# Kernel optimization log

Measured on AMD Instinct MI355X. Metric: run time of the kernel, lower is better.

Reference implementation:

```python
import jax, jax.numpy as jnp
import numpy as np

VOCAB = 50000
OOV = 1000
EMB = 256
H = 512          # decoder hidden
ENC = 512        # 2 * encoder_hidden (bidirectional)
B, S, T = 32, 256, 8
NEG = -1e20


def setup_inputs() -> dict:
    key = jax.random.key(0)
    ks = jax.random.split(key, 16)
    inp = {
        'dec_x': jax.random.randint(ks[0], (B, T), 0, VOCAB),
        'enc_x_with_oov': jax.random.randint(ks[1], (B, S), 0, VOCAB + OOV),
        'enc_len': jax.random.randint(ks[2], (B,), 64, S + 1),
        'enc_output': jax.random.normal(ks[3], (B, S, ENC), jnp.float32),
        'enc_h': jax.random.normal(ks[4], (B, H), jnp.float32),
        'enc_c': jax.random.normal(ks[5], (B, H), jnp.float32),
        'batch_size': B,
        'dec_len': T,
        # learned parameters
        'embedding': jax.random.normal(ks[6], (VOCAB, EMB), jnp.float32) * 0.02,
        'lstm_k': jax.random.normal(ks[7], (EMB, 4 * H), jnp.float32) * 0.02,
        'lstm_r': jax.random.normal(ks[8], (H, 4 * H), jnp.float32) * 0.02,
        'lstm_b': jnp.zeros((4 * H,), jnp.float32),
        'attn_w': jax.random.normal(ks[9], (H, ENC), jnp.float32) * 0.02,
        'out_w': jax.random.normal(ks[10], (ENC + H, H), jnp.float32) * 0.02,
        'out_b': jnp.zeros((H,), jnp.float32),
        'gen_w': jax.random.normal(ks[11], (H, VOCAB), jnp.float32) * 0.02,
        'copy_w': jax.random.normal(ks[12], (ENC, H), jnp.float32) * 0.02,
        'copy_b': jnp.zeros((H,), jnp.float32),
    }
    return inp


def _lstm(x, h0, c0, Wk, Wr, b):
    # x: [B, T, E] -> hidden states [B, T, H], final (h, c)
    def step(carry, x_t):
        h, c = carry
        z = x_t @ Wk + h @ Wr + b  # [B, 4H]
        i, f, g, o = jnp.split(z, 4, axis=-1)
        c = jax.nn.sigmoid(f) * c + jax.nn.sigmoid(i) * jnp.tanh(g)
        h = jax.nn.sigmoid(o) * jnp.tanh(c)
        return (h, c), h
    (h, c), hs = jax.lax.scan(step, (h0, c0), jnp.swapaxes(x, 0, 1))
    return jnp.swapaxes(hs, 0, 1), h, c


def reference(dec_x, enc_x_with_oov, enc_len, enc_output, enc_h, enc_c,
              batch_size, dec_len, embedding, lstm_k, lstm_r, lstm_b,
              attn_w, out_w, out_b, gen_w, copy_w, copy_b):
    mask = jnp.arange(S) < enc_len[:, None]          # [B, S] True = keep

    embed_dec = embedding[dec_x]                      # [B, T, E]
    hidden, state_h, state_c = _lstm(embed_dec, enc_h, enc_c, lstm_k, lstm_r, lstm_b)

    # attention ('general' score)
    q = hidden @ attn_w                               # [B, T, ENC]
    scores = jnp.einsum('bte,bse->bts', q, enc_output)
    scores = jnp.where(mask[:, None, :], scores, NEG)
    attn = jax.nn.softmax(scores, axis=2)             # [B, T, S]
    context = jnp.einsum('bts,bse->bte', attn, enc_output)
    attn_out = jnp.tanh(jnp.concatenate([context, hidden], axis=-1) @ out_w + out_b)  # [B, T, H]

    # generation scores, padded with tiny constant for OOV slots
    gen = jnp.exp(attn_out @ gen_w)                   # [B, T, VOCAB]
    gen = jnp.pad(gen, ((0, 0), (0, 0), (0, OOV)), constant_values=1e-10)

    # copy scores scattered into extended vocab
    k = jnp.tanh(enc_output @ copy_w + copy_b)        # [B, S, H]
    cs = jnp.einsum('bsh,bth->bts', k, attn_out)      # [B, T, S]
    cs = jnp.exp(jnp.where(mask[:, None, :], cs, NEG))
    Vt = VOCAB + OOV
    copy_vocab = jnp.zeros((B, T, Vt), cs.dtype).at[
        jnp.arange(B)[:, None, None],
        jnp.arange(T)[None, :, None],
        enc_x_with_oov[:, None, :],
    ].add(cs)                                         # scatter-add, dup indices sum

    total = gen + copy_vocab
    total_prob = jnp.log(total / jnp.sum(total, axis=2, keepdims=True))
    return total_prob, state_h, state_c
```

## Files before the change

### kernel.cpp

```cpp
#include <hip/hip_runtime.h>
#include <hip/hip_bf16.h>

typedef unsigned short u16;
typedef unsigned int   u32;
typedef __attribute__((ext_vector_type(4))) float f4v;
typedef __attribute__((ext_vector_type(8))) short s8v;
typedef __attribute__((ext_vector_type(4))) unsigned int u4v;

#define NB   32
#define NS   256
#define NT   8
#define NH   512
#define NENC 512
#define NEMB 256
#define NVOC 50000
#define NVT  51000

__device__ __forceinline__ float bf2f(u16 u){ return __uint_as_float(((u32)u)<<16); }
__device__ __forceinline__ u16 f2bf(float f){
  u32 x = __float_as_uint(f);
  return (u16)((x + 0x7fffu + ((x>>16)&1u)) >> 16);
}
__device__ __forceinline__ s8v ld_frag16(const u16* p){
  union{ s8v v; u4v u; } t;
  t.u = *(const u4v*)p;
  return t.v;
}
__device__ __forceinline__ f4v mfma16(s8v a, s8v b, f4v c){
  return __builtin_amdgcn_mfma_f32_16x16x32_bf16(a,b,c,0,0,0);
}
__device__ __forceinline__ float sigm(float x){ return 1.f/(1.f+__expf(-x)); }

__global__ __launch_bounds__(256)
void transpose_cvt(const float* __restrict__ in, u16* __restrict__ out,
                   int K, int N)
{
  in  += (size_t)blockIdx.z * K * N;
  out += (size_t)blockIdx.z * K * N;
  __shared__ u16 tile[32*40];
  const int n0 = blockIdx.x*32, k0 = blockIdx.y*32;
  const int tid = threadIdx.x;
  {
    int r = tid>>3, c4 = tid&7;
    int c = n0 + c4*4;
    if (c+4 > N) c = N-4;
    f4v v = *(const f4v*)(in + (size_t)(k0+r)*N + c);
    uint2 p;
    p.x = (u32)f2bf(v.x) | ((u32)f2bf(v.y)<<16);
    p.y = (u32)f2bf(v.z) | ((u32)f2bf(v.w)<<16);
    *(uint2*)&tile[r*40 + c4*4] = p;
  }
  __syncthreads();
  {
    int r2 = tid>>3, kc = tid&7;
    int n = n0 + r2;
    if (n < N){
      u16 e[4];
      #pragma unroll
      for (int j=0; j<4; ++j) e[j] = tile[(kc*4+j)*40 + r2];
      *(uint2*)(out + (size_t)n*K + k0 + kc*4) = *(uint2*)e;
    }
  }
}

__global__ __launch_bounds__(256)
void cvt_bf16(const float* __restrict__ src, u16* __restrict__ dst){
  int i = (blockIdx.x*256 + threadIdx.x) * 4;
  f4v v = *(const f4v*)(src + i);
  uint2 p;
  p.x = (u32)f2bf(v.x) | ((u32)f2bf(v.y)<<16);
  p.y = (u32)f2bf(v.z) | ((u32)f2bf(v.w)<<16);
  *(uint2*)(dst + i) = p;
}

template<int BM, int BN, int EPI, bool ABF16, bool AGATHER, bool MXA>
__global__ __launch_bounds__(256)
void gemm_bt(const void* __restrict__ Av, const u16* __restrict__ Bt,
             float* __restrict__ C, const int* __restrict__ a_idx,
             const float* __restrict__ bias, float* __restrict__ rowsum,
             int K, int lda, int ldc, int nlim)
{
  constexpr int LDT = 40;
  constexpr int PA  = ABF16 ? BM/64 : BM/32;
  constexpr int PB  = BN/64;
  __shared__ u16 Al[2][BM*LDT];
  __shared__ u16 Bl[2][BN*LDT];
  const int tid  = threadIdx.x;
  const int lane = tid & 63;
  const int wave = tid >> 6;
  const int m0 = (MXA ? blockIdx.x : blockIdx.y) * BM;
  const int n0 = (MXA ? blockIdx.y : blockIdx.x) * BN;
  constexpr int TM = BM/32;
  constexpr int TN = BN/32;
  const int wm = (wave>>1)*(BM/2);
  const int wn = (wave&1)*(BN/2);
  const int q  = lane >> 4;
  const int ln = lane & 15;

  const u16*  aS16[PA];
  const float* aS32[PA];
  int aOff[PA];
  if (ABF16){
    const u16* Ag = (const u16*)Av;
    #pragma unroll
    for (int p=0; p<PA; ++p){
      int el = tid + p*256, row = el>>2, ck = el&3;
      aS16[p] = Ag + (size_t)(m0+row)*lda + ck*8;
      aS32[p] = nullptr;
      aOff[p] = row*LDT + ck*8;
    }
  } else {
    const float* Ag = (const float*)Av;
    #pragma unroll
    for (int p=0; p<PA; ++p){
      int el = tid + p*256, row = el>>3, ck = el&7;
      int grow = AGATHER ? a_idx[m0+row] : (m0+row);
      aS32[p] = Ag + (size_t)grow*lda + ck*4;
      aS16[p] = nullptr;
      aOff[p] = row*LDT + ck*4;
    }
  }
  const u16* bS[PB];
  int bOff[PB];
  #pragma unroll
  for (int p=0; p<PB; ++p){
    int el = tid + p*256, row = el>>2, ck = el&3;
    int nr = n0 + row; if (nr >= nlim) nr = nlim-1;
    bS[p]   = Bt + (size_t)nr*K + ck*8;
    bOff[p] = row*LDT + ck*8;
  }

  f4v acc[TM][TN];
  #pragma unroll
  for (int im=0; im<TM; ++im)
    #pragma unroll
    for (int in=0; in<TN; ++in) acc[im][in] = 0.f;

  u4v aR[PA]; f4v aF[PA]; u4v bR[PB];
  if (ABF16){
    #pragma unroll
    for (int p=0; p<PA; ++p) aR[p] = *(const u4v*)(aS16[p]);
  } else {
    #pragma unroll
    for (int p=0; p<PA; ++p) aF[p] = *(const f4v*)(aS32[p]);
  }
  #pragma unroll
  for (int p=0; p<PB; ++p) bR[p] = *(const u4v*)(bS[p]);

  const int KB = K >> 5;
  int cur = 0;
  for (int kb=0; kb<KB; ++kb){
    if (ABF16){
      #pragma unroll
      for (int p=0; p<PA; ++p) *(u4v*)&Al[cur][aOff[p]] = aR[p];
    } else {
      #pragma unroll
      for (int p=0; p<PA; ++p){
        uint2 pk;
        pk.x = (u32)f2bf(aF[p].x) | ((u32)f2bf(aF[p].y)<<16);
        pk.y = (u32)f2bf(aF[p].z) | ((u32)f2bf(aF[p].w)<<16);
        *(uint2*)&Al[cur][aOff[p]] = pk;
      }
    }
    #pragma unroll
    for (int p=0; p<PB; ++p) *(u4v*)&Bl[cur][bOff[p]] = bR[p];
    if (kb+1 < KB){
      const int ko = (kb+1)*32;
      if (ABF16){
        #pragma unroll
        for (int p=0; p<PA; ++p) aR[p] = *(const u4v*)(aS16[p] + ko);
      } else {
        #pragma unroll
        for (int p=0; p<PA; ++p) aF[p] = *(const f4v*)(aS32[p] + ko);
      }
      #pragma unroll
      for (int p=0; p<PB; ++p) bR[p] = *(const u4v*)(bS[p] + ko);
    }
    __syncthreads();
    s8v af[TM], bfr[TN];
    #pragma unroll
    for (int im=0; im<TM; ++im)
      af[im] = ld_frag16(&Al[cur][(wm+im*16+ln)*LDT + q*8]);
    #pragma unroll
    for (int in=0; in<TN; ++in)
      bfr[in] = ld_frag16(&Bl[cur][(wn+in*16+ln)*LDT + q*8]);
    #pragma unroll
    for (int im=0; im<TM; ++im)
      #pragma unroll
      for (int in=0; in<TN; ++in)
        acc[im][in] = mfma16(af[im], bfr[in], acc[im][in]);
    cur ^= 1;
  }

  #pragma unroll
  for (int im=0; im<TM; ++im){
    const int rbase = m0 + wm + im*16 + q*4;
    #pragma unroll
    for (int in=0; in<TN; ++in){
      const int col = n0 + wn + in*16 + ln;
      if (EPI == 0){
        #pragma unroll
        for (int r=0; r<4; ++r)
          C[(size_t)(rbase+r)*ldc + col] = acc[im][in][r];
      } else if (EPI == 1){
        float bb = bias[col];
        u16* Cb = (u16*)C;
        #pragma unroll
        for (int r=0; r<4; ++r)
          Cb[(size_t)(rbase+r)*ldc + col] = f2bf(tanhf(acc[im][in][r] + bb));
      } else if (EPI == 3){
        u16* Cb = (u16*)C;
        #pragma unroll
        for (int r=0; r<4; ++r)
          Cb[(size_t)(rbase+r)*ldc + col] = f2bf(acc[im][in][r]);
      }
    }
  }
}

__global__ __launch_bounds__(256, 3)
void gen_nat(const u16* __restrict__ A,
             const float* __restrict__ W,
             float* __restrict__ outp)
{
  constexpr int LDT = 40;
  __shared__ u16 Al[2][256*LDT];
  __shared__ u16 Bl[2][64*LDT];
  const int tid  = threadIdx.x;
  const int lane = tid & 63, wave = tid >> 6;
  const int q = lane >> 4, ln = lane & 15;
  const int wm = (wave >> 1) * 128;
  const int wn = (wave & 1) * 32;
  const int n0 = blockIdx.x * 64;

  const int arow = tid >> 2, ack = (tid & 3) * 8;
  const int kp = tid >> 4;
  const int nw = tid & 15;
  int bcol = n0 + nw*4; if (bcol > NVOC-4) bcol = NVOC-4;
  const float* w0 = W + (size_t)(2*kp)  *NVOC + bcol;
  const float* w1 = W + (size_t)(2*kp+1)*NVOC + bcol;
  const int bLoff = (nw*4)*LDT + kp*2;
  const size_t CH = (size_t)32*NVOC;

  f4v acc[8][2];
  #pragma unroll
  for (int im=0; im<8; ++im){ acc[im][0] = 0.f; acc[im][1] = 0.f; }

  u4v aA[4], aB[4];
  f4v b0A, b1A, b0B, b1B;
  #pragma unroll
  for (int p=0; p<4; ++p)
    aA[p] = *(const u4v*)(A + (size_t)(arow + p*64)*NH + ack);
  b0A = *(const f4v*)(w0);
  b1A = *(const f4v*)(w1);
  #pragma unroll
  for (int p=0; p<4; ++p)
    aB[p] = *(const u4v*)(A + (size_t)(arow + p*64)*NH + 32 + ack);
  b0B = *(const f4v*)(w0 + CH);
  b1B = *(const f4v*)(w1 + CH);

  for (int kb=0; kb<16; kb+=2){
    #pragma unroll
    for (int p=0; p<4; ++p) *(u4v*)&Al[0][(arow + p*64)*LDT + ack] = aA[p];
    #pragma unroll
    for (int i=0; i<4; ++i){
      u32 v = (u32)f2bf(b0A[i]) | ((u32)f2bf(b1A[i])<<16);
      *(u32*)&Bl[0][bLoff + i*LDT] = v;
    }
    if (kb+2 < 16){
      #pragma unroll
      for (int p=0; p<4; ++p)
        aA[p] = *(const u4v*)(A + (size_t)(arow + p*64)*NH + (kb+2)*32 + ack);
      b0A = *(const f4v*)(w0 + (size_t)(kb+2)*CH);
      b1A = *(const f4v*)(w1 + (size_t)(kb+2)*CH);
    }
    __syncthreads();
    {
      s8v bf0 = ld_frag16(&Bl[0][(wn + ln)*LDT + q*8]);
      s8v bf1 = ld_frag16(&Bl[0][(wn + 16 + ln)*LDT + q*8]);
      #pragma unroll
      for (int im=0; im<8; ++im){
        s8v af = ld_frag16(&Al[0][(wm + im*16 + ln)*LDT + q*8]);
        acc[im][0] = mfma16(af, bf0, acc[im][0]);
        acc[im][1] = mfma16(af, bf1, acc[im][1]);
      }
    }
    #pragma unroll
    for (int p=0; p<4; ++p) *(u4v*)&Al[1][(arow + p*64)*LDT + ack] = aB[p];
    #pragma unroll
    for (int i=0; i<4; ++i){
      u32 v = (u32)f2bf(b0B[i]) | ((u32)f2bf(b1B[i])<<16);
      *(u32*)&Bl[1][bLoff + i*LDT] = v;
    }
    if (kb+3 < 16){
      #pragma unroll
      for (int p=0; p<4; ++p)
        aB[p] = *(const u4v*)(A + (size_t)(arow + p*64)*NH + (kb+3)*32 + ack);
      b0B = *(const f4v*)(w0 + (size_t)(kb+3)*CH);
      b1B = *(const f4v*)(w1 + (size_t)(kb+3)*CH);
    }
    __syncthreads();
    {
      s8v bf0 = ld_frag16(&Bl[1][(wn + ln)*LDT + q*8]);
      s8v bf1 = ld_frag16(&Bl[1][(wn + 16 + ln)*LDT + q*8]);
      #pragma unroll
      for (int im=0; im<8; ++im){
        s8v af = ld_frag16(&Al[1][(wm + im*16 + ln)*LDT + q*8]);
        acc[im][0] = mfma16(af, bf0, acc[im][0]);
        acc[im][1] = mfma16(af, bf1, acc[im][1]);
      }
    }
  }

  #pragma unroll
  for (int im=0; im<8; ++im){
    const int rbase = wm + im*16 + q*4;
    #pragma unroll
    for (int in=0; in<2; ++in){
      const int col = n0 + wn + in*16 + ln;
      if (col < NVT){
        #pragma unroll
        for (int r=0; r<4; ++r){
          float v = (col < NVOC) ? __expf(acc[im][in][r]) : 1e-10f;
          outp[(size_t)(rbase+r)*NVT + col] = v;
        }
      }
    }
  }
}

__global__ __launch_bounds__(256)
void lstm_step2(const u16* __restrict__ wrT, const float* __restrict__ xk,
                const float* __restrict__ bias, const u16* __restrict__ hb_in,
                u16* __restrict__ hb_out, float* __restrict__ c_cur,
                float* __restrict__ concat, float* __restrict__ out_h,
                float* __restrict__ out_c, int t)
{
  const int tid = threadIdx.x, lane = tid & 63, g = tid >> 6;
  const int q = lane >> 4, ln = lane & 15;
  const int j0 = blockIdx.x * 16;

  f4v acc0 = 0.f, acc1 = 0.f;
  const u16* bp = wrT + (size_t)(g*NH + j0 + ln)*NH;
  const u16* a0 = hb_in + (size_t)ln*NH;
  const u16* a1 = hb_in + (size_t)(16+ln)*NH;
  #pragma unroll 4
  for (int kb=0; kb<16; ++kb){
    s8v bf  = ld_frag16(bp + kb*32 + q*8);
    s8v af0 = ld_frag16(a0 + kb*32 + q*8);
    s8v af1 = ld_frag16(a1 + kb*32 + q*8);
    acc0 = mfma16(af0, bf, acc0);
    acc1 = mfma16(af1, bf, acc1);
  }

  __shared__ float zs[4][32][17];
  #pragma unroll
  for (int r=0; r<4; ++r){
    zs[g][q*4+r][ln]    = acc0[r];
    zs[g][16+q*4+r][ln] = acc1[r];
  }
  __syncthreads();

  #pragma unroll
  for (int pp=0; pp<2; ++pp){
    int pair = tid + pp*256;
    int b = pair >> 4, jj = pair & 15;
    int j = j0 + jj;
    const float* xr = xk + (size_t)(b*NT+t)*2048;
    float zi = zs[0][b][jj] + xr[j]        + bias[j];
    float zf = zs[1][b][jj] + xr[NH+j]     + bias[NH+j];
    float zg = zs[2][b][jj] + xr[2*NH+j]   + bias[2*NH+j];
    float zo = zs[3][b][jj] + xr[3*NH+j]   + bias[3*NH+j];
    float c = sigm(zf)*c_cur[(size_t)b*NH+j] + sigm(zi)*tanhf(zg);
    float h = sigm(zo)*tanhf(c);
    c_cur[(size_t)b*NH+j] = c;
    hb_out[(size_t)b*NH+j] = f2bf(h);
    concat[(size_t)(b*NT+t)*1024 + 512 + j] = h;
    if (t == NT-1){ out_h[(size_t)b*NH+j] = h; out_c[(size_t)b*NH+j] = c; }
  }
}

__global__ __launch_bounds__(512)
void attn_sm(const u16* __restrict__ q_bf,
             const u16* __restrict__ enc_bf,
             const int* __restrict__ enc_len,
             float* __restrict__ at_p)
{
  const int b = blockIdx.x;
  __shared__ u16 Al[16*520];
  __shared__ float at[8][256];
  const int tid = threadIdx.x;
  for (int i=tid; i<16*64; i+=512){
    int row = i >> 6, ck = i & 63;
    uint2 v0 = {0u,0u}, v1 = {0u,0u};
    if (row < NT){
      const u16* s = q_bf + ((size_t)(b*NT+row))*NH + ck*8;
      v0 = *(const uint2*)s; v1 = *(const uint2*)(s+4);
    }
    u16* d = &Al[row*520 + ck*8];
    *(uint2*)d = v0; *(uint2*)(d+4) = v1;
  }
  __syncthreads();
  const int wave = tid >> 6, lane = tid & 63;
  const int q = lane >> 4, ln = lane & 15;
  const int len = enc_len[b];
  f4v acc0 = 0.f, acc1 = 0.f;
  const u16* Bg0 = enc_bf + ((size_t)(b*NS + wave*32 + ln))*NENC;
  const u16* Bg1 = enc_bf + ((size_t)(b*NS + wave*32 + 16 + ln))*NENC;
  for (int kb=0; kb<16; ++kb){
    s8v a  = ld_frag16(&Al[ln*520 + kb*32 + q*8]);
    s8v b0 = ld_frag16(Bg0 + kb*32 + q*8);
    s8v b1 = ld_frag16(Bg1 + kb*32 + q*8);
    acc0 = mfma16(a, b0, acc0);
    acc1 = mfma16(a, b1, acc1);
  }
  {
    const int s0 = wave*32 + ln, s1 = s0 + 16;
    const bool m0 = s0 < len, m1 = s1 < len;
    #pragma unroll
    for (int r=0; r<4; ++r){
      int t = q*4 + r;
      if (t < NT){
        at[t][s0] = m0 ? acc0[r] : -3.0e38f;
        at[t][s1] = m1 ? acc1[r] : -3.0e38f;
      }
    }
  }
  __syncthreads();
  {
    float v[4]; float mx = -3.0e38f;
    #pragma unroll
    for (int i=0;i<4;++i){ v[i] = at[wave][lane+64*i]; mx = fmaxf(mx, v[i]); }
    #pragma unroll
    for (int off=1; off<64; off<<=1) mx = fmaxf(mx, __shfl_xor(mx, off, 64));
    float sum = 0.f;
    #pragma unroll
    for (int i=0;i<4;++i){ v[i] = __expf(v[i]-mx); sum += v[i]; }
    #pragma unroll
    for (int off=1; off<64; off<<=1) sum += __shfl_xor(sum, off, 64);
    float inv = 1.f/sum;
    #pragma unroll
    for (int i=0;i<4;++i)
      at_p[((size_t)(b*NT+wave))*NS + lane+64*i] = v[i]*inv;
  }
}

__global__ __launch_bounds__(256)
void attn_ctx2(const float* __restrict__ at_p,
               const u16* __restrict__ encT_bf,
               float* __restrict__ concat)
{
  const int b = blockIdx.x, eb = blockIdx.y;
  __shared__ u16 Al[16*264];
  const int tid = threadIdx.x;
  for (int i=tid; i<16*64; i+=256){
    int row = i >> 6, c4 = i & 63;
    uint2 pk = {0u,0u};
    if (row < NT){
      f4v v = *(const f4v*)(at_p + ((size_t)(b*NT+row))*NS + c4*4);
      pk.x = (u32)f2bf(v.x) | ((u32)f2bf(v.y)<<16);
      pk.y = (u32)f2bf(v.z) | ((u32)f2bf(v.w)<<16);
    }
    *(uint2*)&Al[row*264 + c4*4] = pk;
  }
  __syncthreads();
  const int wave = tid >> 6, lane = tid & 63;
  const int q = lane >> 4, ln = lane & 15;
  const int e = eb*64 + wave*16 + ln;
  f4v acc = 0.f;
  const u16* Bg = encT_bf + ((size_t)(b*NENC + e))*NS;
  for (int kb=0; kb<8; ++kb){
    s8v a  = ld_frag16(&Al[ln*264 + kb*32 + q*8]);
    s8v bb = ld_frag16(Bg + kb*32 + q*8);
    acc = mfma16(a, bb, acc);
  }
  #pragma unroll
  for (int r=0; r<4; ++r){
    int t = q*4 + r;
    if (t < NT) concat[(size_t)(b*NT+t)*1024 + e] = acc[r];
  }
}

__global__ __launch_bounds__(256)
void cs_scatter(const u16* __restrict__ attn_bf, const u16* __restrict__ copy_k,
                const int* __restrict__ enc_x, const int* __restrict__ enc_len,
                float* __restrict__ outp)
{
  const int b  = blockIdx.x >> 2;
  const int sb = blockIdx.x & 3;
  __shared__ u16 Al[16*520];
  const int tid = threadIdx.x;
  for (int i=tid; i<16*64; i+=256){
    int row = i >> 6, ck = i & 63;
    uint2 v0 = {0u,0u}, v1 = {0u,0u};
    if (row < NT){
      const u16* s = attn_bf + ((size_t)(b*NT+row))*NH + ck*8;
      v0 = *(const uint2*)s; v1 = *(const uint2*)(s+4);
    }
    u16* d = &Al[row*520 + ck*8];
    *(uint2*)d = v0; *(uint2*)(d+4) = v1;
  }
  __syncthreads();
  const int wave = tid >> 6, lane = tid & 63;
  const int q = lane >> 4, ln = lane & 15;
  const int s0 = sb*64 + wave*16;
  f4v acc = 0.f;
  const u16* Bg = copy_k + ((size_t)(b*NS + s0 + ln))*NH;
  for (int kb=0; kb<16; ++kb){
    s8v a  = ld_frag16(&Al[ln*520 + kb*32 + q*8]);
    s8v bb = ld_frag16(Bg + kb*32 + q*8);
    acc = mfma16(a, bb, acc);
  }
  const int s = s0 + ln;
  const int len = enc_len[b];
  const int vidx = enc_x[b*NS + s];
  const bool valid = (s < len);
  #pragma unroll
  for (int r=0; r<4; ++r){
    int t = q*4 + r;
    float e = (valid && t < NT) ? __expf(acc[r]) : 0.f;
    if (e != 0.f) atomicAdd(&outp[(size_t)(b*NT+t)*NVT + vidx], e);
  }
}

__global__ __launch_bounds__(256)
void row_reduce_log(const float* __restrict__ outp, float* __restrict__ logsum)
{
  const int r = blockIdx.x;
  const int tid = threadIdx.x;
  const float* p = outp + (size_t)r*NVT;
  float sum = 0.f;
  for (int i4 = tid; i4 < 12750; i4 += 256){
    f4v v = *(const f4v*)(p + i4*4);
    sum += v.x + v.y + v.z + v.w;
  }
  #pragma unroll
  for (int off=1; off<64; off<<=1) sum += __shfl_xor(sum, off, 64);
  __shared__ float ws[4];
  if ((tid & 63) == 0) ws[tid>>6] = sum;
  __syncthreads();
  if (tid == 0) logsum[r] = __logf(ws[0]+ws[1]+ws[2]+ws[3]);
}

__global__ __launch_bounds__(256)
void norm_log(float* __restrict__ outp, const float* __restrict__ logsum){
  const int i4 = blockIdx.x*256 + threadIdx.x;
  if (i4 >= 12750) return;
  const int r = blockIdx.y;
  const float ls = logsum[r];
  float* p = outp + (size_t)r*NVT + i4*4;
  f4v v = *(const f4v*)p;
  v.x = __logf(v.x) - ls;
  v.y = __logf(v.y) - ls;
  v.z = __logf(v.z) - ls;
  v.w = __logf(v.w) - ls;
  *(f4v*)p = v;
}

extern "C" void kernel_launch(void* const* d_in, const int* in_sizes, int n_in,
                              void* d_out, int out_size, void* d_ws, size_t ws_size,
                              hipStream_t stream)
{
  (void)in_sizes; (void)n_in; (void)out_size; (void)ws_size;
  const int*   dec_x      = (const int*)  d_in[0];
  const int*   enc_x      = (const int*)  d_in[1];
  const int*   enc_len    = (const int*)  d_in[2];
  const float* enc_output = (const float*)d_in[3];
  const float* enc_h      = (const float*)d_in[4];
  const float* enc_c      = (const float*)d_in[5];
  const float* embedding  = (const float*)d_in[8];
  const float* lstm_k     = (const float*)d_in[9];
  const float* lstm_r     = (const float*)d_in[10];
  const float* lstm_b     = (const float*)d_in[11];
  const float* attn_w     = (const float*)d_in[12];
  const float* out_w      = (const float*)d_in[13];
  const float* out_b      = (const float*)d_in[14];
  const float* gen_w      = (const float*)d_in[15];
  const float* copy_w     = (const float*)d_in[16];
  const float* copy_b     = (const float*)d_in[17];

  float* outp  = (float*)d_out;
  float* out_h = outp + (size_t)NB*NT*NVT;
  float* out_c = out_h + NB*NH;

  char* ws = (char*)d_ws;
  u16*   wrT     = (u16*)ws;    ws += (size_t)2048*NH*2;
  u16*   lstmkT  = (u16*)ws;    ws += (size_t)2048*NEMB*2;
  u16*   attnT   = (u16*)ws;    ws += (size_t)NENC*NH*2;
  u16*   outT    = (u16*)ws;    ws += (size_t)NH*1024*2;
  u16*   copyT   = (u16*)ws;    ws += (size_t)NH*NENC*2;
  float* xk      = (float*)ws;  ws += (size_t)NB*NT*2048*4;
  u16*   hb0     = (u16*)ws;    ws += (size_t)NB*NH*2;
  u16*   hb1     = (u16*)ws;    ws += (size_t)NB*NH*2;
  float* c_cur   = (float*)ws;  ws += (size_t)NB*NH*4;
  u16*   q_bf    = (u16*)ws;    ws += (size_t)NB*NT*NENC*2;
  float* at_p    = (float*)ws;  ws += (size_t)NB*NT*NS*4;
  float* concat  = (float*)ws;  ws += (size_t)NB*NT*1024*4;
  u16*   attn_bf = (u16*)ws;    ws += (size_t)NB*NT*NH*2;
  u16*   copy_k  = (u16*)ws;    ws += (size_t)NB*NS*NH*2;
  u16*   enc_bf  = (u16*)ws;    ws += (size_t)NB*NS*NENC*2;
  u16*   encT_bf = (u16*)ws;    ws += (size_t)NB*NENC*NS*2;
  float* logsum  = (float*)ws;  ws += NB*NT*4;

  cvt_bf16<<<4096,256,0,stream>>>(enc_output, enc_bf);
  transpose_cvt<<<dim3(16,8,32),256,0,stream>>>(enc_output, encT_bf, NS, NENC);
  transpose_cvt<<<dim3(64,16), 256,0,stream>>>(lstm_r, wrT,    NH,  2048);
  transpose_cvt<<<dim3(64,8),  256,0,stream>>>(lstm_k, lstmkT, NEMB,2048);
  transpose_cvt<<<dim3(16,16), 256,0,stream>>>(attn_w, attnT,  NH,  NENC);
  transpose_cvt<<<dim3(16,32), 256,0,stream>>>(out_w,  outT,   1024,NH);
  transpose_cvt<<<dim3(16,16), 256,0,stream>>>(copy_w, copyT,  NENC,NH);
  cvt_bf16<<<16,256,0,stream>>>(enc_h, hb0);
  hipMemcpyAsync(c_cur, enc_c, NB*NH*4, hipMemcpyDeviceToDevice, stream);

  gemm_bt<64,128,1,true,false,false><<<dim3(4,128),256,0,stream>>>(
      enc_bf, copyT, (float*)copy_k, nullptr, copy_b, nullptr, NENC, NENC, NH, NH);

  gemm_bt<32,64,0,false,true,true><<<dim3(8,32),256,0,stream>>>(
      embedding, lstmkT, xk, dec_x, nullptr, nullptr, NEMB, NEMB, 2048, 2048);

  u16* hb[2] = {hb0, hb1};
  for (int t=0; t<NT; ++t)
    lstm_step2<<<32,256,0,stream>>>(wrT, xk, lstm_b, hb[t&1], hb[(t+1)&1],
                                    c_cur, concat, out_h, out_c, t);

  gemm_bt<32,64,3,false,false,true><<<dim3(8,8),256,0,stream>>>(
      concat + 512, attnT, (float*)q_bf, nullptr, nullptr, nullptr, NH, 1024, NENC, NENC);

  attn_sm<<<32,512,0,stream>>>(q_bf, enc_bf, enc_len, at_p);
  attn_ctx2<<<dim3(32,8),256,0,stream>>>(at_p, encT_bf, concat);

  gemm_bt<32,64,1,false,false,true><<<dim3(8,8),256,0,stream>>>(
      concat, outT, (float*)attn_bf, nullptr, out_b, nullptr, 1024, 1024, NH, NH);

  gen_nat<<<797,256,0,stream>>>(attn_bf, gen_w, outp);

  cs_scatter<<<128,256,0,stream>>>(attn_bf, copy_k, enc_x, enc_len, outp);
  row_reduce_log<<<NB*NT,256,0,stream>>>(outp, logsum);
  norm_log<<<dim3(50,NB*NT),256,0,stream>>>(outp, logsum);
}
```

Measured before the change: 451.6 us.

## Fuse row-sum into gen/copy epilogues, merge weight transposes, drop LDS A staging

```diff
diff --git a/kernel.cpp b/kernel.cpp
--- a/kernel.cpp
+++ b/kernel.cpp
@@ -31,15 +31,11 @@
 }
 __device__ __forceinline__ float sigm(float x){ return 1.f/(1.f+__expf(-x)); }
 
-__global__ __launch_bounds__(256)
-void transpose_cvt(const float* __restrict__ in, u16* __restrict__ out,
-                   int K, int N)
-{
-  in  += (size_t)blockIdx.z * K * N;
-  out += (size_t)blockIdx.z * K * N;
-  __shared__ u16 tile[32*40];
-  const int n0 = blockIdx.x*32, k0 = blockIdx.y*32;
-  const int tid = threadIdx.x;
+__device__ __forceinline__ void transpose_body(const float* in, u16* out,
+                                               int K, int N, int bx, int by,
+                                               int tid, u16* tile)
+{
+  const int n0 = bx*32, k0 = by*32;
   {
     int r = tid>>3, c4 = tid&7;
     int c = n0 + c4*4;
@@ -61,6 +57,35 @@
       *(uint2*)(out + (size_t)n*K + k0 + kc*4) = *(uint2*)e;
     }
   }
+}
+
+__global__ __launch_bounds__(256)
+void transpose_cvt(const float* __restrict__ in, u16* __restrict__ out,
+                   int K, int N)
+{
+  __shared__ u16 tile[32*40];
+  in  += (size_t)blockIdx.z * K * N;
+  out += (size_t)blockIdx.z * K * N;
+  transpose_body(in, out, K, N, blockIdx.x, blockIdx.y, threadIdx.x, tile);
+}
+
+__global__ __launch_bounds__(256)
+void prep_weights(const float* __restrict__ lstm_r, u16* __restrict__ wrT,
+                  const float* __restrict__ lstm_k, u16* __restrict__ lstmkT,
+                  const float* __restrict__ attn_w, u16* __restrict__ attnT,
+                  const float* __restrict__ out_w,  u16* __restrict__ outT,
+                  const float* __restrict__ copy_w, u16* __restrict__ copyT)
+{
+  __shared__ u16 tile[32*40];
+  const int bid = blockIdx.x;
+  const float* in; u16* out; int K, N, nx, lid;
+  if (bid < 1024)      { in=lstm_r; out=wrT;    K=512;  N=2048; nx=64; lid=bid; }
+  else if (bid < 1536) { in=lstm_k; out=lstmkT; K=256;  N=2048; nx=64; lid=bid-1024; }
+  else if (bid < 1792) { in=attn_w; out=attnT;  K=512;  N=512;  nx=16; lid=bid-1536; }
+  else if (bid < 2304) { in=out_w;  out=outT;   K=1024; N=512;  nx=16; lid=bid-1792; }
+  else                 { in=copy_w; out=copyT;  K=512;  N=512;  nx=16; lid=bid-2304; }
+  int bx = lid % nx, by = lid / nx;
+  transpose_body(in, out, K, N, bx, by, threadIdx.x, tile);
 }
 
 __global__ __launch_bounds__(256)
@@ -218,13 +243,12 @@
   }
 }
 
-__global__ __launch_bounds__(256, 3)
+__global__ __launch_bounds__(256, 4)
 void gen_nat(const u16* __restrict__ A,
              const float* __restrict__ W,
-             float* __restrict__ outp)
+             float* __restrict__ outp, float* __restrict__ rowsum)
 {
   constexpr int LDT = 40;
-  __shared__ u16 Al[2][256*LDT];
   __shared__ u16 Bl[2][64*LDT];
   const int tid  = threadIdx.x;
   const int lane = tid & 63, wave = tid >> 6;
@@ -233,44 +257,37 @@
   const int wn = (wave & 1) * 32;
   const int n0 = blockIdx.x * 64;
 
-  const int arow = tid >> 2, ack = (tid & 3) * 8;
   const int kp = tid >> 4;
   const int nw = tid & 15;
   int bcol = n0 + nw*4; if (bcol > NVOC-4) bcol = NVOC-4;
   const float* w0 = W + (size_t)(2*kp)  *NVOC + bcol;
   const float* w1 = W + (size_t)(2*kp+1)*NVOC + bcol;
-  const int bLoff = (nw*4)*LDT + kp*2;
+  const int bRow = nw*4;
   const size_t CH = (size_t)32*NVOC;
 
+  const u16* aP[8];
+  #pragma unroll
+  for (int im=0; im<8; ++im)
+    aP[im] = A + (size_t)(wm + im*16 + ln)*NH;
+
   f4v acc[8][2];
   #pragma unroll
   for (int im=0; im<8; ++im){ acc[im][0] = 0.f; acc[im][1] = 0.f; }
 
-  u4v aA[4], aB[4];
   f4v b0A, b1A, b0B, b1B;
-  #pragma unroll
-  for (int p=0; p<4; ++p)
-    aA[p] = *(const u4v*)(A + (size_t)(arow + p*64)*NH + ack);
   b0A = *(const f4v*)(w0);
   b1A = *(const f4v*)(w1);
-  #pragma unroll
-  for (int p=0; p<4; ++p)
-    aB[p] = *(const u4v*)(A + (size_t)(arow + p*64)*NH + 32 + ack);
   b0B = *(const f4v*)(w0 + CH);
   b1B = *(const f4v*)(w1 + CH);
 
   for (int kb=0; kb<16; kb+=2){
     #pragma unroll
-    for (int p=0; p<4; ++p) *(u4v*)&Al[0][(arow + p*64)*LDT + ack] = aA[p];
-    #pragma unroll
-    for (int i=0; i<4; ++i){
+    for (int j=0; j<4; ++j){
+      int i = (j + nw) & 3;
       u32 v = (u32)f2bf(b0A[i]) | ((u32)f2bf(b1A[i])<<16);
-      *(u32*)&Bl[0][bLoff + i*LDT] = v;
+      *(u32*)&Bl[0][(bRow + i)*LDT + kp*2] = v;
     }
     if (kb+2 < 16){
-      #pragma unroll
-      for (int p=0; p<4; ++p)
-        aA[p] = *(const u4v*)(A + (size_t)(arow + p*64)*NH + (kb+2)*32 + ack);
       b0A = *(const f4v*)(w0 + (size_t)(kb+2)*CH);
       b1A = *(const f4v*)(w1 + (size_t)(kb+2)*CH);
     }
@@ -280,22 +297,18 @@
       s8v bf1 = ld_frag16(&Bl[0][(wn + 16 + ln)*LDT + q*8]);
       #pragma unroll
       for (int im=0; im<8; ++im){
-        s8v af = ld_frag16(&Al[0][(wm + im*16 + ln)*LDT + q*8]);
+        s8v af = ld_frag16(aP[im] + kb*32 + q*8);
         acc[im][0] = mfma16(af, bf0, acc[im][0]);
         acc[im][1] = mfma16(af, bf1, acc[im][1]);
       }
     }
     #pragma unroll
-    for (int p=0; p<4; ++p) *(u4v*)&Al[1][(arow + p*64)*LDT + ack] = aB[p];
-    #pragma unroll
-    for (int i=0; i<4; ++i){
+    for (int j=0; j<4; ++j){
+      int i = (j + nw) & 3;
       u32 v = (u32)f2bf(b0B[i]) | ((u32)f2bf(b1B[i])<<16);
-      *(u32*)&Bl[1][bLoff + i*LDT] = v;
+      *(u32*)&Bl[1][(bRow + i)*LDT + kp*2] = v;
     }
     if (kb+3 < 16){
-      #pragma unroll
-      for (int p=0; p<4; ++p)
-        aB[p] = *(const u4v*)(A + (size_t)(arow + p*64)*NH + (kb+3)*32 + ack);
       b0B = *(const f4v*)(w0 + (size_t)(kb+3)*CH);
       b1B = *(const f4v*)(w1 + (size_t)(kb+3)*CH);
     }
@@ -305,7 +318,7 @@
       s8v bf1 = ld_frag16(&Bl[1][(wn + 16 + ln)*LDT + q*8]);
       #pragma unroll
       for (int im=0; im<8; ++im){
-        s8v af = ld_frag16(&Al[1][(wm + im*16 + ln)*LDT + q*8]);
+        s8v af = ld_frag16(aP[im] + (kb+1)*32 + q*8);
         acc[im][0] = mfma16(af, bf0, acc[im][0]);
         acc[im][1] = mfma16(af, bf1, acc[im][1]);
       }
@@ -315,16 +328,30 @@
   #pragma unroll
   for (int im=0; im<8; ++im){
     const int rbase = wm + im*16 + q*4;
+    float rs[4] = {0.f,0.f,0.f,0.f};
     #pragma unroll
     for (int in=0; in<2; ++in){
       const int col = n0 + wn + in*16 + ln;
       if (col < NVT){
+        bool ok = col < NVOC;
         #pragma unroll
         for (int r=0; r<4; ++r){
-          float v = (col < NVOC) ? __expf(acc[im][in][r]) : 1e-10f;
-          outp[(size_t)(rbase+r)*NVT + col] = v;
+          float e = ok ? __expf(acc[im][in][r]) : 1e-10f;
+          outp[(size_t)(rbase+r)*NVT + col] = e;
+          if (ok) rs[r] += e;
         }
       }
+    }
+    #pragma unroll
+    for (int off=1; off<16; off<<=1){
+      rs[0] += __shfl_xor(rs[0], off, 64);
+      rs[1] += __shfl_xor(rs[1], off, 64);
+      rs[2] += __shfl_xor(rs[2], off, 64);
+      rs[3] += __shfl_xor(rs[3], off, 64);
+    }
+    if (ln == 0){
+      #pragma unroll
+      for (int r=0; r<4; ++r) atomicAdd(&rowsum[rbase+r], rs[r]);
     }
   }
 }
@@ -484,7 +511,7 @@
 __global__ __launch_bounds__(256)
 void cs_scatter(const u16* __restrict__ attn_bf, const u16* __restrict__ copy_k,
                 const int* __restrict__ enc_x, const int* __restrict__ enc_len,
-                float* __restrict__ outp)
+                float* __restrict__ outp, float* __restrict__ rowsum)
 {
   const int b  = blockIdx.x >> 2;
   const int sb = blockIdx.x & 3;
@@ -515,31 +542,33 @@
   const int len = enc_len[b];
   const int vidx = enc_x[b*NS + s];
   const bool valid = (s < len);
+  float rs[4];
   #pragma unroll
   for (int r=0; r<4; ++r){
     int t = q*4 + r;
     float e = (valid && t < NT) ? __expf(acc[r]) : 0.f;
+    rs[r] = e;
     if (e != 0.f) atomicAdd(&outp[(size_t)(b*NT+t)*NVT + vidx], e);
   }
-}
-
-__global__ __launch_bounds__(256)
-void row_reduce_log(const float* __restrict__ outp, float* __restrict__ logsum)
-{
-  const int r = blockIdx.x;
-  const int tid = threadIdx.x;
-  const float* p = outp + (size_t)r*NVT;
-  float sum = 0.f;
-  for (int i4 = tid; i4 < 12750; i4 += 256){
-    f4v v = *(const f4v*)(p + i4*4);
-    sum += v.x + v.y + v.z + v.w;
-  }
-  #pragma unroll
-  for (int off=1; off<64; off<<=1) sum += __shfl_xor(sum, off, 64);
-  __shared__ float ws[4];
-  if ((tid & 63) == 0) ws[tid>>6] = sum;
-  __syncthreads();
-  if (tid == 0) logsum[r] = __logf(ws[0]+ws[1]+ws[2]+ws[3]);
+  #pragma unroll
+  for (int off=1; off<16; off<<=1){
+    rs[0] += __shfl_xor(rs[0], off, 64);
+    rs[1] += __shfl_xor(rs[1], off, 64);
+    rs[2] += __shfl_xor(rs[2], off, 64);
+    rs[3] += __shfl_xor(rs[3], off, 64);
+  }
+  if (ln == 0){
+    #pragma unroll
+    for (int r=0; r<4; ++r){
+      int t = q*4 + r;
+      if (t < NT) atomicAdd(&rowsum[b*NT+t], rs[r]);
+    }
+  }
+}
+
+__global__ void log_rowsum(float* rowsum){
+  int i = threadIdx.x;
+  rowsum[i] = __logf(rowsum[i] + 1e-7f);
 }
 
 __global__ __launch_bounds__(256)
@@ -600,15 +629,14 @@
   u16*   copy_k  = (u16*)ws;    ws += (size_t)NB*NS*NH*2;
   u16*   enc_bf  = (u16*)ws;    ws += (size_t)NB*NS*NENC*2;
   u16*   encT_bf = (u16*)ws;    ws += (size_t)NB*NENC*NS*2;
-  float* logsum  = (float*)ws;  ws += NB*NT*4;
+  float* rowsum  = (float*)ws;  ws += NB*NT*4;
+
+  hipMemsetAsync(rowsum, 0, NB*NT*4, stream);
 
   cvt_bf16<<<4096,256,0,stream>>>(enc_output, enc_bf);
   transpose_cvt<<<dim3(16,8,32),256,0,stream>>>(enc_output, encT_bf, NS, NENC);
-  transpose_cvt<<<dim3(64,16), 256,0,stream>>>(lstm_r, wrT,    NH,  2048);
-  transpose_cvt<<<dim3(64,8),  256,0,stream>>>(lstm_k, lstmkT, NEMB,2048);
-  transpose_cvt<<<dim3(16,16), 256,0,stream>>>(attn_w, attnT,  NH,  NENC);
-  transpose_cvt<<<dim3(16,32), 256,0,stream>>>(out_w,  outT,   1024,NH);
-  transpose_cvt<<<dim3(16,16), 256,0,stream>>>(copy_w, copyT,  NENC,NH);
+  prep_weights<<<2560,256,0,stream>>>(lstm_r, wrT, lstm_k, lstmkT,
+                                      attn_w, attnT, out_w, outT, copy_w, copyT);
   cvt_bf16<<<16,256,0,stream>>>(enc_h, hb0);
   hipMemcpyAsync(c_cur, enc_c, NB*NH*4, hipMemcpyDeviceToDevice, stream);
 
@@ -632,9 +660,9 @@
   gemm_bt<32,64,1,false,false,true><<<dim3(8,8),256,0,stream>>>(
       concat, outT, (float*)attn_bf, nullptr, out_b, nullptr, 1024, 1024, NH, NH);
 
-  gen_nat<<<797,256,0,stream>>>(attn_bf, gen_w, outp);
-
-  cs_scatter<<<128,256,0,stream>>>(attn_bf, copy_k, enc_x, enc_len, outp);
-  row_reduce_log<<<NB*NT,256,0,stream>>>(outp, logsum);
-  norm_log<<<dim3(50,NB*NT),256,0,stream>>>(outp, logsum);
-}
+  gen_nat<<<797,256,0,stream>>>(attn_bf, gen_w, outp, rowsum);
+
+  cs_scatter<<<128,256,0,stream>>>(attn_bf, copy_k, enc_x, enc_len, outp, rowsum);
+  log_rowsum<<<1,NB*NT,0,stream>>>(rowsum);
+  norm_log<<<dim3(50,NB*NT),256,0,stream>>>(outp, rowsum);
+}
```

Measured after the change: 639.5 us. +41.6%, slower.
